# Kernel tuning notes

Hardware: AMD Instinct MI355X
Metric: run time of the kernel (lower is better)

The kernel has to match this reference:

```python
import jax, jax.numpy as jnp
import numpy as np

SHAPES = [(76, 76), (38, 38), (19, 19), (1, 20)]  # 3 feature levels + task-token pseudo-level
D, HEADS, NLVL, NPTS = 256, 8, 4, 4
DH = D // HEADS
NLAYERS = 6
B = 2
S = sum(h * w for h, w in SHAPES)  # 7601


def _ref_points():
    # valid_ratios == 1 (no padding) -> normalized pixel-center grid per level, concatenated. [S,2] (x,y)
    refs = []
    for H, W in SHAPES:
        ry, rx = jnp.meshgrid(jnp.linspace(0.5, H - 0.5, H) / H,
                              jnp.linspace(0.5, W - 0.5, W) / W, indexing='ij')
        refs.append(jnp.stack([rx.ravel(), ry.ravel()], -1))
    return jnp.concatenate(refs, 0)


def _layer_norm(x, g, b):
    m = x.mean(-1, keepdims=True)
    v = ((x - m) ** 2).mean(-1, keepdims=True)
    return (x - m) * jax.lax.rsqrt(v + 1e-5) * g + b


def _bilinear(val_l, locx, locy, H, W):
    # val_l: [B, H*W, HEADS, DH]; locx/locy: [B,Q,HEADS,P] normalized coords.
    # grid_sample semantics: align_corners=False, zero padding.
    v = val_l.transpose(0, 2, 1, 3)  # [B,Hh,HW,DH]
    x = locx * W - 0.5
    y = locy * H - 0.5
    x0 = jnp.floor(x)
    y0 = jnp.floor(y)
    wx1 = x - x0
    wy1 = y - y0

    def corner(xi, yi, w):
        valid = ((xi >= 0) & (xi <= W - 1) & (yi >= 0) & (yi <= H - 1)).astype(v.dtype)
        idx = (jnp.clip(yi, 0, H - 1) * W + jnp.clip(xi, 0, W - 1)).astype(jnp.int32)
        idx_t = idx.transpose(0, 2, 1, 3)  # [B,Hh,Q,P]
        Bq, Hh, Q, P = idx_t.shape
        g = jnp.take_along_axis(v, idx_t.reshape(Bq, Hh, Q * P)[..., None], axis=2)
        g = g.reshape(Bq, Hh, Q, P, DH)
        return g * (w * valid).transpose(0, 2, 1, 3)[..., None]

    return (corner(x0, y0, (1 - wx1) * (1 - wy1)) + corner(x0 + 1, y0, wx1 * (1 - wy1))
            + corner(x0, y0 + 1, (1 - wx1) * wy1) + corner(x0 + 1, y0 + 1, wx1 * wy1))


def _msdeform(q, x, ref, Woff, boff, Wa, ba, Wv, bv, Wo, bo):
    Bq, Sq, _ = x.shape
    value = (x @ Wv + bv).reshape(Bq, Sq, HEADS, DH)
    off = (q @ Woff + boff).reshape(Bq, Sq, HEADS, NLVL, NPTS, 2)
    attn = jax.nn.softmax((q @ Wa + ba).reshape(Bq, Sq, HEADS, NLVL * NPTS), -1)
    attn = attn.reshape(Bq, Sq, HEADS, NLVL, NPTS)
    acc = jnp.zeros((Bq, HEADS, Sq, DH), x.dtype)
    start = 0
    for l, (H, W) in enumerate(SHAPES):
        n = H * W
        loc = ref[None, :, None, None, :] + off[:, :, :, l] / jnp.asarray([W, H], x.dtype)
        samp = _bilinear(value[:, start:start + n], loc[..., 0], loc[..., 1], H, W)  # [B,Hh,S,P,DH]
        a = attn[:, :, :, l].transpose(0, 2, 1, 3)  # [B,Hh,S,P]
        acc = acc + (samp * a[..., None]).sum(3)
        start += n
    return acc.transpose(0, 2, 1, 3).reshape(Bq, Sq, D) @ Wo + bo


def reference(src0, src1, src2, pos0, pos1, pos2, task_encoding, task_pos_enc, level_embed,
              W_off, b_off, W_attn, b_attn, W_val, b_val, W_out, b_out,
              W1, b1, W2, b2, g1, beta1, g2, beta2):
    srcs, poss = [src0, src1, src2], [pos0, pos1, pos2]
    sf, pf = [], []
    for l in range(3):
        Bq, C, H, W = srcs[l].shape
        sf.append(srcs[l].reshape(Bq, C, H * W).transpose(0, 2, 1))
        pf.append(poss[l].reshape(Bq, C, H * W).transpose(0, 2, 1) + level_embed[l])
    sf.append(task_encoding)
    pf.append(jnp.broadcast_to(task_pos_enc[None], task_encoding.shape))
    x = jnp.concatenate(sf, 1)   # [B,S,D]
    pos = jnp.concatenate(pf, 1)
    ref = _ref_points()
    for i in range(NLAYERS):
        q = x + pos
        x = _layer_norm(x + _msdeform(q, x, ref, W_off[i], b_off[i], W_attn[i], b_attn[i],
                                      W_val[i], b_val[i], W_out[i], b_out[i]), g1[i], beta1[i])
        x = _layer_norm(x + jax.nn.relu(x @ W1[i] + b1[i]) @ W2[i] + b2[i], g2[i], beta2[i])
    return x


def setup_inputs() -> dict:
    key = jax.random.key(0)
    ks = jax.random.split(key, 20)
    d = {}
    for i, (H, W) in enumerate(SHAPES[:3]):
        d[f'src{i}'] = jax.random.normal(ks[i], (B, D, H, W), jnp.float32)
        d[f'pos{i}'] = jax.random.normal(ks[3 + i], (B, D, H, W), jnp.float32) * 0.1
    d['task_encoding'] = jax.random.normal(ks[6], (B, 20, D), jnp.float32)
    d['task_pos_enc'] = jax.random.normal(ks[7], (20, D), jnp.float32) * 0.1
    d['level_embed'] = jax.random.normal(ks[8], (NLVL, D), jnp.float32) * 0.1

    def w(k, shape, s=0.02):
        return jax.random.normal(k, shape, jnp.float32) * s

    d['W_off'] = w(ks[9], (NLAYERS, D, HEADS * NLVL * NPTS * 2), 0.01)
    d['b_off'] = w(ks[10], (NLAYERS, HEADS * NLVL * NPTS * 2), 0.2)
    d['W_attn'] = w(ks[11], (NLAYERS, D, HEADS * NLVL * NPTS))
    d['b_attn'] = jnp.zeros((NLAYERS, HEADS * NLVL * NPTS), jnp.float32)
    d['W_val'] = w(ks[12], (NLAYERS, D, D))
    d['b_val'] = jnp.zeros((NLAYERS, D), jnp.float32)
    d['W_out'] = w(ks[13], (NLAYERS, D, D))
    d['b_out'] = jnp.zeros((NLAYERS, D), jnp.float32)
    d['W1'] = w(ks[14], (NLAYERS, D, 2048))
    d['b1'] = jnp.zeros((NLAYERS, 2048), jnp.float32)
    d['W2'] = w(ks[15], (NLAYERS, 2048, D))
    d['b2'] = jnp.zeros((NLAYERS, D), jnp.float32)
    d['g1'] = jnp.ones((NLAYERS, D), jnp.float32)
    d['beta1'] = jnp.zeros((NLAYERS, D), jnp.float32)
    d['g2'] = jnp.ones((NLAYERS, D), jnp.float32)
    d['beta2'] = jnp.zeros((NLAYERS, D), jnp.float32)
    return d
```

## Files before the change

kernel.cpp:

```cpp
#include <hip/hip_runtime.h>

#define S_TOT 7601
#define BATCH 2
#define BM (BATCH * S_TOT)
#define DMODEL 256

typedef unsigned short bf16;
typedef __attribute__((ext_vector_type(8))) short v8s;
typedef __attribute__((ext_vector_type(4))) float v4f;

__device__ __forceinline__ float b2f(bf16 u) {
    union { unsigned int i; float f; } v;
    v.i = ((unsigned int)u) << 16;
    return v.f;
}
__device__ __forceinline__ bf16 f2b(float f) {
    union { unsigned int i; float f; } v;
    v.f = f;
    unsigned int r = v.i + 0x7FFFu + ((v.i >> 16) & 1u);
    return (bf16)(r >> 16);
}
__device__ __forceinline__ float ldin(const void* p, size_t i, int isf32) {
    return isf32 ? ((const float*)p)[i] : b2f(((const bf16*)p)[i]);
}

#define GLDS16(gp, lp)                                                          \
    __builtin_amdgcn_global_load_lds(                                           \
        (const __attribute__((address_space(1))) unsigned int*)(gp),            \
        (__attribute__((address_space(3))) unsigned int*)(lp), 16, 0, 0)

__device__ __forceinline__ void xcd_remap(int& bx, int& by) {
    int gx = gridDim.x, gy = gridDim.y;
    int nwg = gx * gy;
    int lin = blockIdx.y * gx + blockIdx.x;
    int q = nwg >> 3, r = nwg & 7;
    int xcd = lin & 7, idx = lin >> 3;
    int lin2 = (xcd < r ? xcd * (q + 1) : r * (q + 1) + (xcd - r) * q) + idx;
    bx = lin2 % gx;
    by = lin2 / gx;
}

__global__ void detect_dtype(const unsigned short* __restrict__ src, int* __restrict__ flag) {
    __shared__ int cnt;
    if (threadIdx.x == 0) cnt = 0;
    __syncthreads();
    int local = 0;
    for (int i = threadIdx.x; i < 16384; i += 256) {
        unsigned int e = (src[i] >> 7) & 0xFFu;
        if (e >= 143u) local++;
    }
    atomicAdd(&cnt, local);
    __syncthreads();
    if (threadIdx.x == 0) *flag = (cnt > 200) ? 1 : 0;
}

__global__ void __launch_bounds__(256) pack_level(const void* __restrict__ src,
                                                  const void* __restrict__ pin,
                                                  const void* __restrict__ lemb, int lrow,
                                                  float* __restrict__ x,
                                                  bf16* __restrict__ pout,
                                                  int HW, int start,
                                                  const int* __restrict__ flag) {
    int isf32 = *flag;
    int i = blockIdx.x * 256 + threadIdx.x;
    int total = BATCH * HW * 256;
    if (i >= total) return;
    int c = i & 255;
    int t = i >> 8;
    int s = t % HW;
    int b = t / HW;
    size_t src_idx = ((size_t)b * 256 + c) * HW + s;
    float sv = ldin(src, src_idx, isf32);
    float pv = ldin(pin, src_idx, isf32) + ldin(lemb, (size_t)lrow * 256 + c, isf32);
    size_t o = ((size_t)b * S_TOT + start + s) * 256 + c;
    x[o] = sv;
    pout[o] = f2b(pv);
}

__global__ void __launch_bounds__(256) pack_task(const void* __restrict__ te,
                                                 const void* __restrict__ tpe,
                                                 float* __restrict__ x,
                                                 bf16* __restrict__ pout,
                                                 const int* __restrict__ flag) {
    int isf32 = *flag;
    int i = blockIdx.x * 256 + threadIdx.x;
    int total = BATCH * 20 * 256;
    if (i >= total) return;
    int c = i & 255;
    int t = (i >> 8) % 20;
    int b = (i >> 8) / 20;
    size_t o = ((size_t)b * S_TOT + 7581 + t) * 256 + c;
    x[o] = ldin(te, ((size_t)b * 20 + t) * 256 + c, isf32);
    pout[o] = f2b(ldin(tpe, (size_t)t * 256 + c, isf32));
}

__global__ void __launch_bounds__(256) make_ref(float* __restrict__ ref) {
    int s = blockIdx.x * 256 + threadIdx.x;
    if (s >= S_TOT) return;
    int H, W, st;
    if (s < 5776)      { H = 76; W = 76; st = 0; }
    else if (s < 7220) { H = 38; W = 38; st = 5776; }
    else if (s < 7581) { H = 19; W = 19; st = 7220; }
    else               { H = 1;  W = 20; st = 7581; }
    int r = s - st;
    int i = r / W, j = r % W;
    ref[s * 2 + 0] = (j + 0.5f) / (float)W;
    ref[s * 2 + 1] = (i + 0.5f) / (float)H;
}

__global__ void __launch_bounds__(256) cast_out(const float* __restrict__ x,
                                                void* __restrict__ o, int n,
                                                const int* __restrict__ flag) {
    int isf32 = *flag;
    int i = blockIdx.x * 256 + threadIdx.x;
    if (i >= n) return;
    if (isf32) ((float*)o)[i] = x[i];
    else       ((bf16*)o)[i] = f2b(x[i]);
}

__global__ void __launch_bounds__(256) cvt_xq(const float* __restrict__ x,
                                              const bf16* __restrict__ pos,
                                              bf16* __restrict__ xb,
                                              bf16* __restrict__ qb, int n4) {
    int i = blockIdx.x * 256 + threadIdx.x;
    if (i >= n4) return;
    float4 xv = ((const float4*)x)[i];
    ushort4 pv = ((const ushort4*)pos)[i];
    ushort4 xo, qo;
    xo.x = f2b(xv.x); xo.y = f2b(xv.y); xo.z = f2b(xv.z); xo.w = f2b(xv.w);
    qo.x = f2b(xv.x + b2f(pv.x));
    qo.y = f2b(xv.y + b2f(pv.y));
    qo.z = f2b(xv.z + b2f(pv.z));
    qo.w = f2b(xv.w + b2f(pv.w));
    ((ushort4*)xb)[i] = xo;
    ((ushort4*)qb)[i] = qo;
}

__global__ void __launch_bounds__(256) transpose_all(const void* __restrict__ Wv,
                                                     const void* __restrict__ Woff,
                                                     const void* __restrict__ Wa,
                                                     const void* __restrict__ Wo,
                                                     const void* __restrict__ W1,
                                                     const void* __restrict__ W2,
                                                     bf16* __restrict__ Wvt,
                                                     bf16* __restrict__ Wqt,
                                                     bf16* __restrict__ Wot,
                                                     bf16* __restrict__ W1t,
                                                     bf16* __restrict__ W2t,
                                                     int L0, const int* __restrict__ flag) {
    int isf32 = *flag;
    int L = (L0 >= 0) ? L0 : (int)blockIdx.y;
    size_t dl = (L0 >= 0) ? 0 : (size_t)blockIdx.y;
    int t = blockIdx.x;
    const void* src; bf16* dst; int K, N; size_t woff; int rowoff = 0;
    if (t < 64)        { src = Wv;   dst = Wvt + dl * 65536;  K = 256;  N = 256;  woff = (size_t)L * 65536; }
    else if (t < 128)  { src = Woff; dst = Wqt + dl * 98304;  K = 256;  N = 256;  woff = (size_t)L * 65536;  t -= 64; }
    else if (t < 160)  { src = Wa;   dst = Wqt + dl * 98304;  K = 256;  N = 128;  woff = (size_t)L * 32768;  rowoff = 256; t -= 128; }
    else if (t < 224)  { src = Wo;   dst = Wot + dl * 65536;  K = 256;  N = 256;  woff = (size_t)L * 65536;  t -= 160; }
    else if (t < 736)  { src = W1;   dst = W1t + dl * 524288; K = 256;  N = 2048; woff = (size_t)L * 524288; t -= 224; }
    else               { src = W2;   dst = W2t + dl * 524288; K = 2048; N = 256;  woff = (size_t)L * 524288; t -= 736; }
    int ntx = N >> 5;
    int tk = (t / ntx) * 32;
    int tn = (t % ntx) * 32;
    __shared__ float tl[32][33];
    int r = threadIdx.x >> 3;
    int c4 = (threadIdx.x & 7) * 4;
#pragma unroll
    for (int i = 0; i < 4; ++i)
        tl[r][c4 + i] = ldin(src, woff + (size_t)(tk + r) * N + tn + c4 + i, isf32);
    __syncthreads();
#pragma unroll
    for (int i = 0; i < 4; ++i)
        dst[(size_t)(tn + r + rowoff) * K + tk + c4 + i] = f2b(tl[c4 + i][r]);
}

__global__ void __launch_bounds__(256) mfma_gemm(const bf16* __restrict__ A,
                                                 const bf16* __restrict__ Wt,
                                                 const void* __restrict__ bias, size_t boff,
                                                 bf16* __restrict__ C,
                                                 int M, int N, int K, int relu,
                                                 const int* __restrict__ flag) {
    int isf32 = *flag;
    __shared__ __align__(16) char smem[128 * 136 * 2];
    bf16* As = (bf16*)smem;
    bf16* Bs = (bf16*)smem + 8192;
    bf16* Cs = (bf16*)smem;
    int tid = threadIdx.x;
    int lane = tid & 63, wave = tid >> 6;
    int wm = (wave & 1) << 6, wn = (wave >> 1) << 6;
    int bx, by;
    xcd_remap(bx, by);
    int bm = by * 128, bn = bx * 128;
    int q = lane >> 4, l15 = lane & 15;

    v4f acc[4][4];
#pragma unroll
    for (int i = 0; i < 4; ++i)
#pragma unroll
        for (int j = 0; j < 4; ++j) acc[i][j] = (v4f){0.f, 0.f, 0.f, 0.f};

    int r0 = tid >> 2, r1 = r0 + 64;
    int oct = (tid & 3) * 8;
    int am0 = bm + r0; if (am0 >= M) am0 = M - 1;
    int am1 = bm + r1; if (am1 >= M) am1 = M - 1;
    const bf16* ag0 = A + (size_t)am0 * K + oct;
    const bf16* ag1 = A + (size_t)am1 * K + oct;
    const bf16* bg0 = Wt + (size_t)(bn + r0) * K + oct;
    const bf16* bg1 = Wt + (size_t)(bn + r1) * K + oct;
    bf16* lA0 = As + tid * 8;
    bf16* lA1 = As + (tid + 256) * 8;
    bf16* lA2 = As + 4096 + tid * 8;
    bf16* lA3 = As + 4096 + (tid + 256) * 8;
    bf16* lB0 = Bs + tid * 8;
    bf16* lB1 = Bs + (tid + 256) * 8;
    bf16* lB2 = Bs + 4096 + tid * 8;
    bf16* lB3 = Bs + 4096 + (tid + 256) * 8;

    for (int k0 = 0; k0 < K; k0 += 64) {
        GLDS16(ag0 + k0, lA0);
        GLDS16(ag1 + k0, lA1);
        GLDS16(ag0 + k0 + 32, lA2);
        GLDS16(ag1 + k0 + 32, lA3);
        GLDS16(bg0 + k0, lB0);
        GLDS16(bg1 + k0, lB1);
        GLDS16(bg0 + k0 + 32, lB2);
        GLDS16(bg1 + k0 + 32, lB3);
        __syncthreads();
#pragma unroll
        for (int h = 0; h < 2; ++h) {
            v8s a_frag[4], b_frag[4];
#pragma unroll
            for (int mi = 0; mi < 4; ++mi)
                a_frag[mi] = *(const v8s*)&As[h * 4096 + (wm + mi * 16 + l15) * 32 + q * 8];
#pragma unroll
            for (int ni = 0; ni < 4; ++ni)
                b_frag[ni] = *(const v8s*)&Bs[h * 4096 + (wn + ni * 16 + l15) * 32 + q * 8];
#pragma unroll
            for (int mi = 0; mi < 4; ++mi)
#pragma unroll
                for (int ni = 0; ni < 4; ++ni)
                    acc[mi][ni] = __builtin_amdgcn_mfma_f32_16x16x32_bf16(
                        a_frag[mi], b_frag[ni], acc[mi][ni], 0, 0, 0);
        }
        __syncthreads();
    }

#pragma unroll
    for (int ni = 0; ni < 4; ++ni) {
        int cn = wn + ni * 16 + l15;
        float bv = ldin(bias, boff + bn + cn, isf32);
#pragma unroll
        for (int mi = 0; mi < 4; ++mi) {
#pragma unroll
            for (int r = 0; r < 4; ++r) {
                float v = acc[mi][ni][r] + bv;
                if (relu) v = fmaxf(v, 0.f);
                Cs[(wm + mi * 16 + q * 4 + r) * 136 + cn] = f2b(v);
            }
        }
    }
    __syncthreads();
    {
        int row = tid >> 1, half = tid & 1;
        int gm = bm + row;
        if (gm < M) {
            const bf16* srcp = Cs + row * 136 + half * 64;
            bf16* dstp = C + (size_t)gm * N + bn + half * 64;
#pragma unroll
            for (int i = 0; i < 8; ++i)
                *(uint4*)(dstp + i * 8) = *(const uint4*)(srcp + i * 8);
        }
    }
}

__global__ void __launch_bounds__(256) mfma_gemm64(const bf16* __restrict__ A,
                                                   const bf16* __restrict__ Wt,
                                                   const void* __restrict__ bias, size_t boff,
                                                   bf16* __restrict__ C,
                                                   int M, int N, int K, int relu,
                                                   const int* __restrict__ flag) {
    int isf32 = *flag;
    __shared__ __align__(16) char smem[16384];
    bf16* As = (bf16*)smem;
    bf16* Bs = (bf16*)smem + 4096;
    bf16* Cs = (bf16*)smem;
    int tid = threadIdx.x;
    int lane = tid & 63, wave = tid >> 6;
    int wm = (wave & 1) * 32, wn = (wave >> 1) * 32;
    int bx, by;
    xcd_remap(bx, by);
    int bm = by * 64, bn = bx * 64;
    int q = lane >> 4, l15 = lane & 15;

    v4f acc[2][2];
#pragma unroll
    for (int i = 0; i < 2; ++i)
#pragma unroll
        for (int j = 0; j < 2; ++j) acc[i][j] = (v4f){0.f, 0.f, 0.f, 0.f};

    int srow = tid >> 2;
    int oct = (tid & 3) * 8;
    int am = bm + srow; if (am >= M) am = M - 1;
    const bf16* arow = A + (size_t)am * K + oct;
    const bf16* brow = Wt + (size_t)(bn + srow) * K + oct;
    bf16* lA0 = As + tid * 8;
    bf16* lA1 = As + 2048 + tid * 8;
    bf16* lB0 = Bs + tid * 8;
    bf16* lB1 = Bs + 2048 + tid * 8;

    for (int k0 = 0; k0 < K; k0 += 64) {
        GLDS16(arow + k0, lA0);
        GLDS16(arow + k0 + 32, lA1);
        GLDS16(brow + k0, lB0);
        GLDS16(brow + k0 + 32, lB1);
        __syncthreads();
#pragma unroll
        for (int h = 0; h < 2; ++h) {
            v8s a_frag[2], b_frag[2];
#pragma unroll
            for (int mi = 0; mi < 2; ++mi)
                a_frag[mi] = *(const v8s*)&As[h * 2048 + (wm + mi * 16 + l15) * 32 + q * 8];
#pragma unroll
            for (int ni = 0; ni < 2; ++ni)
                b_frag[ni] = *(const v8s*)&Bs[h * 2048 + (wn + ni * 16 + l15) * 32 + q * 8];
#pragma unroll
            for (int mi = 0; mi < 2; ++mi)
#pragma unroll
                for (int ni = 0; ni < 2; ++ni)
                    acc[mi][ni] = __builtin_amdgcn_mfma_f32_16x16x32_bf16(
                        a_frag[mi], b_frag[ni], acc[mi][ni], 0, 0, 0);
        }
        __syncthreads();
    }

#pragma unroll
    for (int ni = 0; ni < 2; ++ni) {
        int cn = wn + ni * 16 + l15;
        float bv = ldin(bias, boff + bn + cn, isf32);
#pragma unroll
        for (int mi = 0; mi < 2; ++mi) {
#pragma unroll
            for (int r = 0; r < 4; ++r) {
                float v = acc[mi][ni][r] + bv;
                if (relu) v = fmaxf(v, 0.f);
                Cs[(wm + mi * 16 + q * 4 + r) * 72 + cn] = f2b(v);
            }
        }
    }
    __syncthreads();
    {
        int row = tid >> 2, seg = tid & 3;
        int gm = bm + row;
        if (gm < M) {
            const bf16* srcp = Cs + row * 72 + seg * 16;
            bf16* dstp = C + (size_t)gm * N + bn + seg * 16;
            *(uint4*)(dstp) = *(const uint4*)(srcp);
            *(uint4*)(dstp + 8) = *(const uint4*)(srcp + 8);
        }
    }
}

__global__ void __launch_bounds__(256) mfma_gemm64_q(const bf16* __restrict__ A,
                                                     const bf16* __restrict__ Wt,
                                                     const void* __restrict__ bias0, size_t boff0,
                                                     const void* __restrict__ bias1, size_t boff1,
                                                     bf16* __restrict__ out0,
                                                     bf16* __restrict__ out1,
                                                     int M, int K,
                                                     const int* __restrict__ flag) {
    int isf32 = *flag;
    __shared__ __align__(16) char smem[16384];
    bf16* As = (bf16*)smem;
    bf16* Bs = (bf16*)smem + 4096;
    bf16* Cs = (bf16*)smem;
    int tid = threadIdx.x;
    int lane = tid & 63, wave = tid >> 6;
    int wm = (wave & 1) * 32, wn = (wave >> 1) * 32;
    int bx, by;
    xcd_remap(bx, by);
    int bm = by * 64, bn = bx * 64;
    int q = lane >> 4, l15 = lane & 15;

    v4f acc[2][2];
#pragma unroll
    for (int i = 0; i < 2; ++i)
#pragma unroll
        for (int j = 0; j < 2; ++j) acc[i][j] = (v4f){0.f, 0.f, 0.f, 0.f};

    int srow = tid >> 2;
    int oct = (tid & 3) * 8;
    int am = bm + srow; if (am >= M) am = M - 1;
    const bf16* arow = A + (size_t)am * K + oct;
    const bf16* brow = Wt + (size_t)(bn + srow) * K + oct;
    bf16* lA0 = As + tid * 8;
    bf16* lA1 = As + 2048 + tid * 8;
    bf16* lB0 = Bs + tid * 8;
    bf16* lB1 = Bs + 2048 + tid * 8;

    for (int k0 = 0; k0 < K; k0 += 64) {
        GLDS16(arow + k0, lA0);
        GLDS16(arow + k0 + 32, lA1);
        GLDS16(brow + k0, lB0);
        GLDS16(brow + k0 + 32, lB1);
        __syncthreads();
#pragma unroll
        for (int h = 0; h < 2; ++h) {
            v8s a_frag[2], b_frag[2];
#pragma unroll
            for (int mi = 0; mi < 2; ++mi)
                a_frag[mi] = *(const v8s*)&As[h * 2048 + (wm + mi * 16 + l15) * 32 + q * 8];
#pragma unroll
            for (int ni = 0; ni < 2; ++ni)
                b_frag[ni] = *(const v8s*)&Bs[h * 2048 + (wn + ni * 16 + l15) * 32 + q * 8];
#pragma unroll
            for (int mi = 0; mi < 2; ++mi)
#pragma unroll
                for (int ni = 0; ni < 2; ++ni)
                    acc[mi][ni] = __builtin_amdgcn_mfma_f32_16x16x32_bf16(
                        a_frag[mi], b_frag[ni], acc[mi][ni], 0, 0, 0);
        }
        __syncthreads();
    }

    int isOff = (bn < 256);
    bf16* outp = isOff ? out0 : out1;
    int outN = isOff ? 256 : 128;
    int colbase = isOff ? bn : bn - 256;
    const void* bptr = isOff ? bias0 : bias1;
    size_t bofs = isOff ? boff0 : boff1;

#pragma unroll
    for (int ni = 0; ni < 2; ++ni) {
        int cn = wn + ni * 16 + l15;
        float bv = ldin(bptr, bofs + colbase + cn, isf32);
#pragma unroll
        for (int mi = 0; mi < 2; ++mi) {
#pragma unroll
            for (int r = 0; r < 4; ++r) {
                Cs[(wm + mi * 16 + q * 4 + r) * 72 + cn] = f2b(acc[mi][ni][r] + bv);
            }
        }
    }
    __syncthreads();
    {
        int row = tid >> 2, seg = tid & 3;
        int gm = bm + row;
        if (gm < M) {
            const bf16* srcp = Cs + row * 72 + seg * 16;
            bf16* dstp = outp + (size_t)gm * outN + colbase + seg * 16;
            *(uint4*)(dstp) = *(const uint4*)(srcp);
            *(uint4*)(dstp + 8) = *(const uint4*)(srcp + 8);
        }
    }
}

template<typename TA, int ADDPOS, int RELU>
__global__ void __launch_bounds__(256) gemm_bias(const TA* __restrict__ A,
                                                 const bf16* __restrict__ Apos,
                                                 const void* __restrict__ W, size_t woff,
                                                 const void* __restrict__ bias, size_t boff,
                                                 bf16* __restrict__ C,
                                                 int M, int N, int K,
                                                 const int* __restrict__ flag) {
    int isf32 = *flag;
    __shared__ float As[16][65];
    __shared__ float Bs[16][65];
    int tid = threadIdx.x;
    int tx = tid & 15;
    int ty = tid >> 4;
    int bm = blockIdx.y * 64;
    int bn = blockIdx.x * 64;
    float acc[4][4] = {};
    for (int k0 = 0; k0 < K; k0 += 16) {
#pragma unroll
        for (int e = 0; e < 4; ++e) {
            int idx = tid + e * 256;
            int mm = idx >> 4;
            int kk = idx & 15;
            int gm = bm + mm;
            float av = 0.f;
            if (gm < M) {
                size_t ai = (size_t)gm * K + k0 + kk;
                if (sizeof(TA) == 4) av = ((const float*)A)[ai];
                else                 av = b2f(((const bf16*)A)[ai]);
                if (ADDPOS) av += b2f(Apos[ai]);
            }
            As[kk][mm] = av;
        }
#pragma unroll
        for (int e = 0; e < 4; ++e) {
            int idx = tid + e * 256;
            int kk = idx >> 6;
            int nn = idx & 63;
            int gn = bn + nn;
            Bs[kk][nn] = (gn < N) ? ldin(W, woff + (size_t)(k0 + kk) * N + gn, isf32) : 0.f;
        }
        __syncthreads();
#pragma unroll
        for (int kk = 0; kk < 16; ++kk) {
            float a[4], b[4];
#pragma unroll
            for (int i = 0; i < 4; ++i) a[i] = As[kk][ty + 16 * i];
#pragma unroll
            for (int j = 0; j < 4; ++j) b[j] = Bs[kk][tx + 16 * j];
#pragma unroll
            for (int i = 0; i < 4; ++i)
#pragma unroll
                for (int j = 0; j < 4; ++j) acc[i][j] += a[i] * b[j];
        }
        __syncthreads();
    }
#pragma unroll
    for (int i = 0; i < 4; ++i) {
        int gm = bm + ty + 16 * i;
        if (gm >= M) continue;
#pragma unroll
        for (int j = 0; j < 4; ++j) {
            int gn = bn + tx + 16 * j;
            if (gn >= N) continue;
            float v = acc[i][j] + ldin(bias, boff + gn, isf32);
            if (RELU) v = fmaxf(v, 0.f);
            C[(size_t)gm * N + gn] = f2b(v);
        }
    }
}

__global__ void __launch_bounds__(256) msdeform_sample4(const bf16* __restrict__ value,
                                                        const bf16* __restrict__ off,
                                                        const bf16* __restrict__ logits,
                                                        const float* __restrict__ refpts,
                                                        bf16* __restrict__ out) {
    __shared__ float sAttn[4 * 128];
    __shared__ int2 sIW[4 * 520];
    const int LH[4] = {76, 38, 19, 1};
    const int LW[4] = {76, 38, 19, 20};
    const int LS[4] = {0, 5776, 7220, 7581};
    int tid = threadIdx.x;
    int m0 = blockIdx.x * 4;

    for (int i = tid; i < 4 * 128; i += 256) {
        int r = i >> 7, li = i & 127;
        int m = m0 + r;
        int mc = (m < BM) ? m : BM - 1;
        sAttn[i] = b2f(logits[(size_t)mc * 128 + li]);
    }
    __syncthreads();
    if (tid < 32) {
        float* g = sAttn + tid * 16;
        float mx = -1e30f;
#pragma unroll
        for (int i = 0; i < 16; ++i) mx = fmaxf(mx, g[i]);
        float e[16], sm = 0.f;
#pragma unroll
        for (int i = 0; i < 16; ++i) { e[i] = __expf(g[i] - mx); sm += e[i]; }
        float inv = 1.f / sm;
#pragma unroll
        for (int i = 0; i < 16; ++i) g[i] = e[i] * inv;
    }
    __syncthreads();
    for (int i = tid; i < 4 * 128; i += 256) {
        int r = i >> 7, oi = i & 127;
        int m = m0 + r;
        int mc = (m < BM) ? m : BM - 1;
        int b = mc / S_TOT;
        int s = mc - b * S_TOT;
        int h = oi >> 4;
        int l = (oi >> 2) & 3;
        int H = LH[l], W = LW[l], st = LS[l];
        float fW = (float)W, fH = (float)H;
        float refx = refpts[s * 2 + 0];
        float refy = refpts[s * 2 + 1];
        ushort2 ov = *(const ushort2*)(off + (size_t)mc * 256 + oi * 2);
        float a = sAttn[r * 128 + oi];
        float xpix = (refx + b2f(ov.x) / fW) * fW - 0.5f;
        float ypix = (refy + b2f(ov.y) / fH) * fH - 0.5f;
        float x0f = floorf(xpix), y0f = floorf(ypix);
        int x0 = (int)x0f, y0 = (int)y0f;
        float wx1 = xpix - x0f, wy1 = ypix - y0f;
        float wx0 = 1.f - wx1, wy0 = 1.f - wy1;
        int vb = b * (S_TOT * 256) + h * 32;
        int base = r * 520 + h * 65 + (oi & 15) * 4;
#pragma unroll
        for (int c = 0; c < 4; ++c) {
            int cx = c & 1, cy = c >> 1;
            int xi = x0 + cx, yi = y0 + cy;
            float w = (cx ? wx1 : wx0) * (cy ? wy1 : wy0) * a;
            bool valid = (xi >= 0) && (xi <= W - 1) && (yi >= 0) && (yi <= H - 1);
            int xic = min(max(xi, 0), W - 1), yic = min(max(yi, 0), H - 1);
            int2 d;
            d.x = vb + (st + yic * W + xic) * 256;
            d.y = __float_as_int(valid ? w : 0.f);
            sIW[base + c] = d;
        }
    }
    __syncthreads();
    int r = tid >> 6, u = tid & 63;
    int h = u >> 3, d4 = (u & 7) * 4;
    int m = m0 + r;
    int cb = r * 520 + h * 65;
    float acc0 = 0.f, acc1 = 0.f, acc2 = 0.f, acc3 = 0.f;
#pragma unroll 8
    for (int c = 0; c < 64; ++c) {
        int2 p = sIW[cb + c];
        float w = __int_as_float(p.y);
        ushort4 v = *(const ushort4*)(value + p.x + d4);
        acc0 += w * b2f(v.x);
        acc1 += w * b2f(v.y);
        acc2 += w * b2f(v.z);
        acc3 += w * b2f(v.w);
    }
    if (m < BM) {
        ushort4 o;
        o.x = f2b(acc0); o.y = f2b(acc1); o.z = f2b(acc2); o.w = f2b(acc3);
        *(ushort4*)(out + (size_t)m * 256 + h * 32 + d4) = o;
    }
}

__global__ void __launch_bounds__(256) residual_ln4(float* __restrict__ x,
                                                    const bf16* __restrict__ y,
                                                    const void* __restrict__ g, size_t goff,
                                                    const void* __restrict__ beta, size_t boff,
                                                    const int* __restrict__ flag,
                                                    bf16* __restrict__ xb,
                                                    const bf16* __restrict__ pos,
                                                    bf16* __restrict__ qb) {
    int isf32 = *flag;
    int tid = threadIdx.x;
    int r = tid >> 6, lane = tid & 63;
    int m = blockIdx.x * 4 + r;
    if (m >= BM) return;
    size_t o = (size_t)m * 256 + lane * 4;
    float4 xv = *(const float4*)(x + o);
    ushort4 yv = *(const ushort4*)(y + o);
    float r0 = xv.x + b2f(yv.x), r1 = xv.y + b2f(yv.y);
    float r2 = xv.z + b2f(yv.z), r3 = xv.w + b2f(yv.w);
    float sum = r0 + r1 + r2 + r3;
#pragma unroll
    for (int ofs = 32; ofs > 0; ofs >>= 1) sum += __shfl_xor(sum, ofs);
    float mean = sum * (1.f / 256.f);
    float d0 = r0 - mean, d1 = r1 - mean, d2 = r2 - mean, d3 = r3 - mean;
    float vv = d0 * d0 + d1 * d1 + d2 * d2 + d3 * d3;
#pragma unroll
    for (int ofs = 32; ofs > 0; ofs >>= 1) vv += __shfl_xor(vv, ofs);
    float rstd = rsqrtf(vv * (1.f / 256.f) + 1e-5f);
    int c = lane * 4;
    float o0 = d0 * rstd * ldin(g, goff + c + 0, isf32) + ldin(beta, boff + c + 0, isf32);
    float o1 = d1 * rstd * ldin(g, goff + c + 1, isf32) + ldin(beta, boff + c + 1, isf32);
    float o2 = d2 * rstd * ldin(g, goff + c + 2, isf32) + ldin(beta, boff + c + 2, isf32);
    float o3 = d3 * rstd * ldin(g, goff + c + 3, isf32) + ldin(beta, boff + c + 3, isf32);
    *(float4*)(x + o) = make_float4(o0, o1, o2, o3);
    if (xb) {
        ushort4 xo;
        xo.x = f2b(o0); xo.y = f2b(o1); xo.z = f2b(o2); xo.w = f2b(o3);
        *(ushort4*)(xb + o) = xo;
    }
    if (qb) {
        ushort4 pv = *(const ushort4*)(pos + o);
        ushort4 qo;
        qo.x = f2b(o0 + b2f(pv.x));
        qo.y = f2b(o1 + b2f(pv.y));
        qo.z = f2b(o2 + b2f(pv.z));
        qo.w = f2b(o3 + b2f(pv.w));
        *(ushort4*)(qb + o) = qo;
    }
}

extern "C" void kernel_launch(void* const* d_in, const int* in_sizes, int n_in,
                              void* d_out, int out_size, void* d_ws, size_t ws_size,
                              hipStream_t stream) {
    (void)in_sizes; (void)n_in; (void)out_size;
    const size_t MS = (size_t)BM * DMODEL;

    char* base = (char*)d_ws;
    int* flag    = (int*)base;    base += 256;
    float* x     = (float*)base;  base += MS * 4;
    bf16* value  = (bf16*)base;   base += MS * 2;
    bf16* attnl  = (bf16*)base;   base += (size_t)BM * 128 * 2;
    bf16* pos    = (bf16*)base;   base += MS * 2;
    bf16* offms  = (bf16*)base;   base += MS * 2;
    bf16* yb     = (bf16*)base;   base += MS * 2;
    size_t base_used = (size_t)(base - (char*)d_ws);

    const size_t SZ_WVT = 65536, SZ_WQT = 98304, SZ_WOT = 65536, SZ_W1T = 524288, SZ_W2T = 524288;
    const size_t WB1 = (SZ_WVT + SZ_WQT + SZ_WOT + SZ_W1T + SZ_W2T) * 2;

    bf16* xb = (bf16*)base;
    size_t needB  = base_used + MS * 2 + WB1 + (size_t)S_TOT * 8 + 1024;
    size_t needBH = ((needB + 255) & ~(size_t)255) + (size_t)BM * 2048 * 2;
    size_t needAH = ((base_used + MS * 2 + 6 * WB1 + (size_t)S_TOT * 8 + 1024 + 255) & ~(size_t)255)
                  + (size_t)BM * 2048 * 2;
    bool FAST = ws_size >= needB;
    bool W6   = ws_size >= needAH;
    int  nL   = W6 ? 6 : 1;

    bf16 *W1t = nullptr, *W2t = nullptr, *Wvt = nullptr, *Wqt = nullptr, *Wot = nullptr;
    float* ref;
    bf16* hiddenF = nullptr;
    bool FULLH = false;
    if (FAST) {
        char* p = (char*)xb + MS * 2;
        Wvt = (bf16*)p;  p += (size_t)nL * SZ_WVT * 2;
        Wqt = (bf16*)p;  p += (size_t)nL * SZ_WQT * 2;
        Wot = (bf16*)p;  p += (size_t)nL * SZ_WOT * 2;
        W1t = (bf16*)p;  p += (size_t)nL * SZ_W1T * 2;
        W2t = (bf16*)p;  p += (size_t)nL * SZ_W2T * 2;
        ref = (float*)p; p += (size_t)S_TOT * 2 * 4;
        size_t used = (size_t)(p - (char*)d_ws);
        used = (used + 255) & ~(size_t)255;
        if (ws_size >= used + (size_t)BM * 2048 * 2) {
            hiddenF = (bf16*)((char*)d_ws + used);
            FULLH = true;
        }
    } else {
        ref = (float*)base;
    }

    bf16* hidden = FULLH ? hiddenF : value;
    const int CH = FULLH ? BM : 2816;

    detect_dtype<<<1, 256, 0, stream>>>((const unsigned short*)d_in[0], flag);

    {
        int HW0 = 76 * 76, HW1 = 38 * 38, HW2 = 19 * 19;
        int n0 = BATCH * HW0 * 256, n1 = BATCH * HW1 * 256, n2 = BATCH * HW2 * 256;
        pack_level<<<(n0 + 255) / 256, 256, 0, stream>>>(d_in[0], d_in[1], d_in[8], 0, x, pos, HW0, 0, flag);
        pack_level<<<(n1 + 255) / 256, 256, 0, stream>>>(d_in[2], d_in[3], d_in[8], 1, x, pos, HW1, 5776, flag);
        pack_level<<<(n2 + 255) / 256, 256, 0, stream>>>(d_in[4], d_in[5], d_in[8], 2, x, pos, HW2, 7220, flag);
        int nt = BATCH * 20 * 256;
        pack_task<<<(nt + 255) / 256, 256, 0, stream>>>(d_in[6], d_in[7], x, pos, flag);
        make_ref<<<(S_TOT + 255) / 256, 256, 0, stream>>>(ref);
    }

    const int GM64 = (BM + 63) / 64;
    const int GR4 = (BM + 3) / 4;
    const int n4 = (int)(MS / 4);

    if (FAST) {
        cvt_xq<<<(n4 + 255) / 256, 256, 0, stream>>>(x, pos, xb, yb, n4);
        if (W6) {
            transpose_all<<<dim3(1248, 6), 256, 0, stream>>>(d_in[13], d_in[9], d_in[11], d_in[15],
                                                             d_in[17], d_in[19],
                                                             Wvt, Wqt, Wot, W1t, W2t, -1, flag);
        }
    }

    for (int L = 0; L < 6; ++L) {
        size_t oW256 = (size_t)L * 256 * 256, ob256 = (size_t)L * 256;
        size_t oW128 = (size_t)L * 256 * 128, ob128 = (size_t)L * 128;
        size_t oW1   = (size_t)L * 256 * 2048, ob1  = (size_t)L * 2048;
        size_t oW2   = (size_t)L * 2048 * 256;

        if (FAST) {
            bf16* WvtL = Wvt + (W6 ? (size_t)L * SZ_WVT : 0);
            bf16* WqtL = Wqt + (W6 ? (size_t)L * SZ_WQT : 0);
            bf16* WotL = Wot + (W6 ? (size_t)L * SZ_WOT : 0);
            bf16* W1tL = W1t + (W6 ? (size_t)L * SZ_W1T : 0);
            bf16* W2tL = W2t + (W6 ? (size_t)L * SZ_W2T : 0);
            if (!W6) {
                transpose_all<<<dim3(1248, 1), 256, 0, stream>>>(d_in[13], d_in[9], d_in[11], d_in[15],
                                                                 d_in[17], d_in[19],
                                                                 Wvt, Wqt, Wot, W1t, W2t, L, flag);
            }
            bf16* qb = yb;
            mfma_gemm64<<<dim3(4, GM64), 256, 0, stream>>>(xb, WvtL, d_in[14], ob256, value, BM, 256, 256, 0, flag);
            mfma_gemm64_q<<<dim3(6, GM64), 256, 0, stream>>>(qb, WqtL, d_in[10], ob256, d_in[12], ob128,
                                                             offms, attnl, BM, 256, flag);

            msdeform_sample4<<<GR4, 256, 0, stream>>>(value, offms, attnl, ref, offms);

            mfma_gemm64<<<dim3(4, GM64), 256, 0, stream>>>(offms, WotL, d_in[16], ob256, yb, BM, 256, 256, 0, flag);
            residual_ln4<<<GR4, 256, 0, stream>>>(x, yb, d_in[21], ob256, d_in[22], ob256, flag, xb, nullptr, nullptr);

            for (int r0 = 0; r0 < BM; r0 += CH) {
                int mc = BM - r0 < CH ? BM - r0 : CH;
                int gmc128 = (mc + 127) / 128;
                int gmc64 = (mc + 63) / 64;
                mfma_gemm<<<dim3(16, gmc128), 256, 0, stream>>>(xb + (size_t)r0 * 256, W1tL, d_in[18], ob1,
                                                                hidden, mc, 2048, 256, 1, flag);
                mfma_gemm64<<<dim3(4, gmc64), 256, 0, stream>>>(hidden, W2tL, d_in[20], ob256,
                                                                yb + (size_t)r0 * 256, mc, 256, 2048, 0, flag);
            }
            residual_ln4<<<GR4, 256, 0, stream>>>(x, yb, d_in[23], ob256, d_in[24], ob256, flag, xb,
                                                  (L < 5) ? pos : nullptr, (L < 5) ? yb : nullptr);
        } else {
            dim3 g256(4, GM64);
            dim3 g128(2, GM64);
            gemm_bias<float, 0, 0><<<g256, 256, 0, stream>>>(x, nullptr, d_in[13], oW256, d_in[14], ob256,
                                                             value, BM, 256, 256, flag);
            gemm_bias<float, 1, 0><<<g256, 256, 0, stream>>>(x, pos, d_in[9], oW256, d_in[10], ob256,
                                                             offms, BM, 256, 256, flag);
            gemm_bias<float, 1, 0><<<g128, 256, 0, stream>>>(x, pos, d_in[11], oW128, d_in[12], ob128,
                                                             attnl, BM, 128, 256, flag);
            msdeform_sample4<<<GR4, 256, 0, stream>>>(value, offms, attnl, ref, offms);
            gemm_bias<bf16, 0, 0><<<g256, 256, 0, stream>>>(offms, nullptr, d_in[15], oW256, d_in[16], ob256,
                                                            yb, BM, 256, 256, flag);
            residual_ln4<<<GR4, 256, 0, stream>>>(x, yb, d_in[21], ob256, d_in[22], ob256, flag, nullptr, nullptr, nullptr);
            for (int r0 = 0; r0 < BM; r0 += CH) {
                int mc = BM - r0 < CH ? BM - r0 : CH;
                dim3 gh(32, (mc + 63) / 64);
                dim3 go(4, (mc + 63) / 64);
                gemm_bias<float, 0, 1><<<gh, 256, 0, stream>>>(x + (size_t)r0 * 256, nullptr, d_in[17], oW1,
                                                               d_in[18], ob1, hidden, mc, 2048, 256, flag);
                gemm_bias<bf16, 0, 0><<<go, 256, 0, stream>>>(hidden, nullptr, d_in[19], oW2, d_in[20], ob256,
                                                              yb + (size_t)r0 * 256, mc, 256, 2048, flag);
            }
            residual_ln4<<<GR4, 256, 0, stream>>>(x, yb, d_in[23], ob256, d_in[24], ob256, flag, nullptr, nullptr, nullptr);
        }
    }

    cast_out<<<((int)MS + 255) / 256, 256, 0, stream>>>(x, d_out, (int)MS, flag);
}
```

Baseline: 1.202 ms.

## Fuse value and query projections into one GEMM launch, deepen K tile

Merges the value projection and the offset/attention projection GEMMs into a single launch whose 10 column blocks pick their A matrix, weights, bias and output by block index. Both 64x64 GEMM kernels now stage 128 K-elements per barrier instead of 64, doubling shared memory to 32 KB and halving the synchronisation count. The softmax over 16 attention logits is spread across 8 lanes per group with shuffle reductions instead of running serially on 32 threads. The larger LDS footprint may cut occupancy.

```diff
diff --git a/kernel.cpp b/kernel.cpp
--- a/kernel.cpp
+++ b/kernel.cpp
@@ -280,9 +280,9 @@
                                                    int M, int N, int K, int relu,
                                                    const int* __restrict__ flag) {
     int isf32 = *flag;
-    __shared__ __align__(16) char smem[16384];
+    __shared__ __align__(16) char smem[32768];
     bf16* As = (bf16*)smem;
-    bf16* Bs = (bf16*)smem + 4096;
+    bf16* Bs = (bf16*)smem + 8192;
     bf16* Cs = (bf16*)smem;
     int tid = threadIdx.x;
     int lane = tid & 63, wave = tid >> 6;
@@ -303,19 +303,16 @@
     int am = bm + srow; if (am >= M) am = M - 1;
     const bf16* arow = A + (size_t)am * K + oct;
     const bf16* brow = Wt + (size_t)(bn + srow) * K + oct;
-    bf16* lA0 = As + tid * 8;
-    bf16* lA1 = As + 2048 + tid * 8;
-    bf16* lB0 = Bs + tid * 8;
-    bf16* lB1 = Bs + 2048 + tid * 8;
-
-    for (int k0 = 0; k0 < K; k0 += 64) {
-        GLDS16(arow + k0, lA0);
-        GLDS16(arow + k0 + 32, lA1);
-        GLDS16(brow + k0, lB0);
-        GLDS16(brow + k0 + 32, lB1);
+
+    for (int k0 = 0; k0 < K; k0 += 128) {
+#pragma unroll
+        for (int h = 0; h < 4; ++h) {
+            GLDS16(arow + k0 + h * 32, As + h * 2048 + tid * 8);
+            GLDS16(brow + k0 + h * 32, Bs + h * 2048 + tid * 8);
+        }
         __syncthreads();
 #pragma unroll
-        for (int h = 0; h < 2; ++h) {
+        for (int h = 0; h < 4; ++h) {
             v8s a_frag[2], b_frag[2];
 #pragma unroll
             for (int mi = 0; mi < 2; ++mi)
@@ -360,25 +357,33 @@
     }
 }
 
-__global__ void __launch_bounds__(256) mfma_gemm64_q(const bf16* __restrict__ A,
-                                                     const bf16* __restrict__ Wt,
-                                                     const void* __restrict__ bias0, size_t boff0,
-                                                     const void* __restrict__ bias1, size_t boff1,
-                                                     bf16* __restrict__ out0,
-                                                     bf16* __restrict__ out1,
-                                                     int M, int K,
-                                                     const int* __restrict__ flag) {
+__global__ void __launch_bounds__(256) mfma_gemm64_vq(const bf16* __restrict__ xb,
+                                                      const bf16* __restrict__ qb,
+                                                      const bf16* __restrict__ Wvt,
+                                                      const bf16* __restrict__ Wqt,
+                                                      const void* __restrict__ bv, size_t obv,
+                                                      const void* __restrict__ bo, size_t obo,
+                                                      const void* __restrict__ ba, size_t oba,
+                                                      bf16* __restrict__ valueo,
+                                                      bf16* __restrict__ offo,
+                                                      bf16* __restrict__ attno,
+                                                      int M, const int* __restrict__ flag) {
+    const int K = 256;
     int isf32 = *flag;
-    __shared__ __align__(16) char smem[16384];
+    __shared__ __align__(16) char smem[32768];
     bf16* As = (bf16*)smem;
-    bf16* Bs = (bf16*)smem + 4096;
+    bf16* Bs = (bf16*)smem + 8192;
     bf16* Cs = (bf16*)smem;
     int tid = threadIdx.x;
     int lane = tid & 63, wave = tid >> 6;
     int wm = (wave & 1) * 32, wn = (wave >> 1) * 32;
     int bx, by;
     xcd_remap(bx, by);
-    int bm = by * 64, bn = bx * 64;
+    int bm = by * 64;
+    int isV = (bx < 4);
+    int bn = isV ? bx * 64 : (bx - 4) * 64;
+    const bf16* A = isV ? xb : qb;
+    const bf16* Wt = isV ? Wvt : Wqt;
     int q = lane >> 4, l15 = lane & 15;
 
     v4f acc[2][2];
@@ -392,19 +397,16 @@
     int am = bm + srow; if (am >= M) am = M - 1;
     const bf16* arow = A + (size_t)am * K + oct;
     const bf16* brow = Wt + (size_t)(bn + srow) * K + oct;
-    bf16* lA0 = As + tid * 8;
-    bf16* lA1 = As + 2048 + tid * 8;
-    bf16* lB0 = Bs + tid * 8;
-    bf16* lB1 = Bs + 2048 + tid * 8;
-
-    for (int k0 = 0; k0 < K; k0 += 64) {
-        GLDS16(arow + k0, lA0);
-        GLDS16(arow + k0 + 32, lA1);
-        GLDS16(brow + k0, lB0);
-        GLDS16(brow + k0 + 32, lB1);
+
+    for (int k0 = 0; k0 < K; k0 += 128) {
+#pragma unroll
+        for (int h = 0; h < 4; ++h) {
+            GLDS16(arow + k0 + h * 32, As + h * 2048 + tid * 8);
+            GLDS16(brow + k0 + h * 32, Bs + h * 2048 + tid * 8);
+        }
         __syncthreads();
 #pragma unroll
-        for (int h = 0; h < 2; ++h) {
+        for (int h = 0; h < 4; ++h) {
             v8s a_frag[2], b_frag[2];
 #pragma unroll
             for (int mi = 0; mi < 2; ++mi)
@@ -422,22 +424,20 @@
         __syncthreads();
     }
 
-    int isOff = (bn < 256);
-    bf16* outp = isOff ? out0 : out1;
-    int outN = isOff ? 256 : 128;
-    int colbase = isOff ? bn : bn - 256;
-    const void* bptr = isOff ? bias0 : bias1;
-    size_t bofs = isOff ? boff0 : boff1;
+    bf16* outp; int outN, colbase; const void* bptr; size_t bofs;
+    if (isV)             { outp = valueo; outN = 256; colbase = bn;       bptr = bv; bofs = obv; }
+    else if (bn < 256)   { outp = offo;   outN = 256; colbase = bn;       bptr = bo; bofs = obo; }
+    else                 { outp = attno;  outN = 128; colbase = bn - 256; bptr = ba; bofs = oba; }
 
 #pragma unroll
     for (int ni = 0; ni < 2; ++ni) {
         int cn = wn + ni * 16 + l15;
-        float bv = ldin(bptr, bofs + colbase + cn, isf32);
+        float bvf = ldin(bptr, bofs + colbase + cn, isf32);
 #pragma unroll
         for (int mi = 0; mi < 2; ++mi) {
 #pragma unroll
             for (int r = 0; r < 4; ++r) {
-                Cs[(wm + mi * 16 + q * 4 + r) * 72 + cn] = f2b(acc[mi][ni][r] + bv);
+                Cs[(wm + mi * 16 + q * 4 + r) * 72 + cn] = f2b(acc[mi][ni][r] + bvf);
             }
         }
     }
@@ -545,17 +545,21 @@
         sAttn[i] = b2f(logits[(size_t)mc * 128 + li]);
     }
     __syncthreads();
-    if (tid < 32) {
-        float* g = sAttn + tid * 16;
-        float mx = -1e30f;
-#pragma unroll
-        for (int i = 0; i < 16; ++i) mx = fmaxf(mx, g[i]);
-        float e[16], sm = 0.f;
-#pragma unroll
-        for (int i = 0; i < 16; ++i) { e[i] = __expf(g[i] - mx); sm += e[i]; }
+    {
+        int g = tid >> 3, j = tid & 7;
+        float* gp = sAttn + g * 16;
+        float e0 = gp[j * 2], e1 = gp[j * 2 + 1];
+        float mx = fmaxf(e0, e1);
+#pragma unroll
+        for (int o = 1; o < 8; o <<= 1) mx = fmaxf(mx, __shfl_xor(mx, o));
+        e0 = __expf(e0 - mx);
+        e1 = __expf(e1 - mx);
+        float sm = e0 + e1;
+#pragma unroll
+        for (int o = 1; o < 8; o <<= 1) sm += __shfl_xor(sm, o);
         float inv = 1.f / sm;
-#pragma unroll
-        for (int i = 0; i < 16; ++i) g[i] = e[i] * inv;
+        gp[j * 2] = e0 * inv;
+        gp[j * 2 + 1] = e1 * inv;
     }
     __syncthreads();
     for (int i = tid; i < 4 * 128; i += 256) {
@@ -686,7 +690,6 @@
 
     bf16* xb = (bf16*)base;
     size_t needB  = base_used + MS * 2 + WB1 + (size_t)S_TOT * 8 + 1024;
-    size_t needBH = ((needB + 255) & ~(size_t)255) + (size_t)BM * 2048 * 2;
     size_t needAH = ((base_used + MS * 2 + 6 * WB1 + (size_t)S_TOT * 8 + 1024 + 255) & ~(size_t)255)
                   + (size_t)BM * 2048 * 2;
     bool FAST = ws_size >= needB;
@@ -762,9 +765,10 @@
                                                                  Wvt, Wqt, Wot, W1t, W2t, L, flag);
             }
             bf16* qb = yb;
-            mfma_gemm64<<<dim3(4, GM64), 256, 0, stream>>>(xb, WvtL, d_in[14], ob256, value, BM, 256, 256, 0, flag);
-            mfma_gemm64_q<<<dim3(6, GM64), 256, 0, stream>>>(qb, WqtL, d_in[10], ob256, d_in[12], ob128,
-                                                             offms, attnl, BM, 256, flag);
+            mfma_gemm64_vq<<<dim3(10, GM64), 256, 0, stream>>>(xb, qb, WvtL, WqtL,
+                                                               d_in[14], ob256, d_in[10], ob256,
+                                                               d_in[12], ob128,
+                                                               value, offms, attnl, BM, flag);
 
             msdeform_sample4<<<GR4, 256, 0, stream>>>(value, offms, attnl, ref, offms);
 
```

After: 1.203 ms. Within noise of the previous version (+0.1%).
